# Optimization experiments

Measured on AMD Instinct MI355X. Metric: run time of the kernel, lower is better.

## Reference

```python
import jax, jax.numpy as jnp
import numpy as np

N_NODES = 50000
N_EDGES = 800000
IN_FEAT = 512
HIDDEN = 64
N_CLASS = 16


def setup_inputs() -> dict:
    key = jax.random.key(0)
    ks = jax.random.split(key, 8)
    x = jax.random.normal(ks[0], (N_NODES, IN_FEAT), dtype=jnp.float32)
    src = jax.random.randint(ks[1], (N_EDGES,), 0, N_NODES, dtype=jnp.int32)
    dst = jax.random.randint(ks[2], (N_EDGES,), 0, N_NODES, dtype=jnp.int32)
    edge_weight = jax.random.uniform(ks[3], (N_EDGES,), dtype=jnp.float32)
    # Glorot-ish init for layer weights (GraphConvolution weight + bias)
    W1 = jax.random.normal(ks[4], (IN_FEAT, HIDDEN), dtype=jnp.float32) * (1.0 / np.sqrt(IN_FEAT))
    b1 = jnp.zeros((HIDDEN,), dtype=jnp.float32)
    W2 = jax.random.normal(ks[5], (HIDDEN, N_CLASS), dtype=jnp.float32) * (1.0 / np.sqrt(HIDDEN))
    b2 = jnp.zeros((N_CLASS,), dtype=jnp.float32)
    return {"x": x, "src": src, "dst": dst, "edge_weight": edge_weight,
            "W1": W1, "b1": b1, "W2": W2, "b2": b2}


def _spmm(src, dst, edge_weight, h):
    # sparse adj @ h via gather + weighted segment_sum over destination nodes
    msgs = h[src] * edge_weight[:, None]          # [E, d]
    return jax.ops.segment_sum(msgs, dst, num_segments=N_NODES)  # [N, d]


def reference(x, src, dst, edge_weight, W1, b1, W2, b2):
    # Layer 1: relu(adj @ (x @ W1) + b1)
    h = _spmm(src, dst, edge_weight, x @ W1) + b1   # [N, HIDDEN]
    h = jax.nn.relu(h)
    # Dropout is identity at inference (predict uses training=False).
    # Layer 2: softmax(adj @ (h @ W2) + b2)
    logits = _spmm(src, dst, edge_weight, h @ W2) + b2  # [N, N_CLASS]
    return jax.nn.softmax(logits, axis=-1)
```

## Files before the change

kernel.cpp:

```cpp
#include <hip/hip_runtime.h>

#define IN_FEAT 512
#define HIDDEN 64
#define N_CLASS 16
#define CAP 64
#define EPT 4

typedef __attribute__((ext_vector_type(8))) short bf16x8;
typedef __attribute__((ext_vector_type(8))) unsigned short ushort8;
typedef __attribute__((ext_vector_type(4))) float f32x4;

struct EdgeRec { int s; float w; };

__device__ inline unsigned short f2bf(float f) {
    union { float f; unsigned int u; } x; x.f = f;
    unsigned int u = x.u + 0x7FFFu + ((x.u >> 16) & 1u);
    return (unsigned short)(u >> 16);
}

__global__ __launch_bounds__(256) void k_init(const float* __restrict__ W1,
                                              unsigned short* __restrict__ bfrag,
                                              int* __restrict__ deg, int n) {
    int bid = blockIdx.x;
    if (bid < 16) {
        int t = bid * 256 + threadIdx.x;
        int l = t & 63;
        int grp = t >> 6;
        int ct = grp & 3, kc = grp >> 2;
        int k0 = kc * 32 + (l >> 4) * 8;
        int col = ct * 16 + (l & 15);
        ushort8 v;
#pragma unroll
        for (int j = 0; j < 8; ++j) v[j] = f2bf(W1[(k0 + j) * HIDDEN + col]);
        ((ushort8*)bfrag)[t] = v;
    } else {
        int i = (bid - 16) * 256 + threadIdx.x;
        if (i < n) deg[i] = 0;
    }
}

__global__ __launch_bounds__(256) void k_fused(const float* __restrict__ x,
                                               const unsigned short* __restrict__ bfrag,
                                               float* __restrict__ h0,
                                               const int* __restrict__ src,
                                               const int* __restrict__ dst,
                                               const float* __restrict__ ew,
                                               int* __restrict__ deg,
                                               EdgeRec* __restrict__ recs,
                                               int n, int E, int gb) {
    int bid = blockIdx.x;
    int gid = bid >> 1;
    if ((bid & 1) == 0) {
        int wid  = gid * 4 + (threadIdx.x >> 6);
        int lane = threadIdx.x & 63;
        int r0 = wid * 16;
        if (r0 >= n) return;
        const float* xp = x + (size_t)(r0 + (lane & 15)) * IN_FEAT + (lane >> 4) * 8;

        bf16x8 afr[16];
#pragma unroll
        for (int kc = 0; kc < 16; ++kc) {
            f32x4 a0 = *(const f32x4*)(xp + kc * 32);
            f32x4 a1 = *(const f32x4*)(xp + kc * 32 + 4);
            bf16x8 a;
#pragma unroll
            for (int j = 0; j < 4; ++j) a[j] = (short)f2bf(a0[j]);
#pragma unroll
            for (int j = 0; j < 4; ++j) a[4 + j] = (short)f2bf(a1[j]);
            afr[kc] = a;
        }

        const bf16x8* B = (const bf16x8*)bfrag;
        f32x4 acc0 = {0,0,0,0}, acc1 = {0,0,0,0}, acc2 = {0,0,0,0}, acc3 = {0,0,0,0};
#pragma unroll
        for (int kc = 0; kc < 16; ++kc) {
            bf16x8 b0 = B[(kc * 4 + 0) * 64 + lane];
            bf16x8 b1 = B[(kc * 4 + 1) * 64 + lane];
            bf16x8 b2 = B[(kc * 4 + 2) * 64 + lane];
            bf16x8 b3 = B[(kc * 4 + 3) * 64 + lane];
            acc0 = __builtin_amdgcn_mfma_f32_16x16x32_bf16(afr[kc], b0, acc0, 0, 0, 0);
            acc1 = __builtin_amdgcn_mfma_f32_16x16x32_bf16(afr[kc], b1, acc1, 0, 0, 0);
            acc2 = __builtin_amdgcn_mfma_f32_16x16x32_bf16(afr[kc], b2, acc2, 0, 0, 0);
            acc3 = __builtin_amdgcn_mfma_f32_16x16x32_bf16(afr[kc], b3, acc3, 0, 0, 0);
        }

        int c = lane & 15;
        int rb = r0 + ((lane >> 4) << 2);
#pragma unroll
        for (int j = 0; j < 4; ++j) {
            float* o = h0 + (size_t)(rb + j) * HIDDEN;
            o[ 0 + c] = acc0[j];
            o[16 + c] = acc1[j];
            o[32 + c] = acc2[j];
            o[48 + c] = acc3[j];
        }
    } else {
        int base = gid * (256 * EPT) + threadIdx.x;
        int  dd[EPT], ss[EPT];
        float ww[EPT];
        bool pp[EPT];
#pragma unroll
        for (int k = 0; k < EPT; ++k) {
            int i = base + k * 256;
            pp[k] = (i < E);
            int j = pp[k] ? i : 0;
            dd[k] = dst[j];
            ss[k] = src[j];
            ww[k] = ew[j];
        }
        int rr[EPT];
#pragma unroll
        for (int k = 0; k < EPT; ++k)
            rr[k] = pp[k] ? atomicAdd(&deg[dd[k]], 1) : CAP;
#pragma unroll
        for (int k = 0; k < EPT; ++k) {
            if (rr[k] < CAP) {
                EdgeRec rec; rec.s = ss[k]; rec.w = ww[k];
                recs[(size_t)dd[k] * CAP + rr[k]] = rec;
            }
        }
    }
}

__global__ __launch_bounds__(256) void k_spmm1g2(const int* __restrict__ deg,
                                                 const EdgeRec* __restrict__ recs,
                                                 const float* __restrict__ h0,
                                                 const float* __restrict__ b1,
                                                 const float* __restrict__ W2,
                                                 float* __restrict__ h2, int n) {
    int wid  = blockIdx.x * 4 + (threadIdx.x >> 6);
    int lane = threadIdx.x & 63;
    if (wid >= n) return;
    int node = __builtin_amdgcn_readfirstlane(wid);
    int cnt = deg[node]; if (cnt > CAP) cnt = CAP;
    const EdgeRec* er = recs + (size_t)node * CAP;

    EdgeRec myr = {0, 0.f};
    if (lane < cnt) myr = er[lane];

    int f  = lane & 15;
    int kb = lane & 48;
    float bias = b1[lane];
    float w2r[16];
#pragma unroll
    for (int j = 0; j < 16; ++j) w2r[j] = W2[(kb + j) * N_CLASS + f];

    float acc = 0.f;
    for (int e = 0; e < cnt; e += 8) {
#define STEP(k)                                              \
        int   s##k = __shfl(myr.s, e + k, 64);               \
        float w##k = __shfl(myr.w, e + k, 64);               \
        bool  p##k = (e + k < cnt);                          \
        s##k = p##k ? s##k : 0;                              \
        w##k = p##k ? w##k : 0.f;                            \
        float g##k = h0[(size_t)s##k * HIDDEN + lane];
        STEP(0) STEP(1) STEP(2) STEP(3) STEP(4) STEP(5) STEP(6) STEP(7)
#undef STEP
        acc = fmaf(w0, g0, acc);
        acc = fmaf(w1, g1, acc);
        acc = fmaf(w2, g2, acc);
        acc = fmaf(w3, g3, acc);
        acc = fmaf(w4, g4, acc);
        acc = fmaf(w5, g5, acc);
        acc = fmaf(w6, g6, acc);
        acc = fmaf(w7, g7, acc);
    }
    float h1v = acc + bias;
    h1v = h1v > 0.f ? h1v : 0.f;

    float sum = 0.f;
#pragma unroll
    for (int j = 0; j < 16; ++j) {
        float hk = __shfl(h1v, kb + j, 64);
        sum = fmaf(hk, w2r[j], sum);
    }
    sum += __shfl_xor(sum, 16, 64);
    sum += __shfl_xor(sum, 32, 64);
    if (lane < 16) h2[(size_t)node * N_CLASS + lane] = sum;
}

__global__ __launch_bounds__(256) void k_spmm2(const int* __restrict__ deg,
                                               const EdgeRec* __restrict__ recs,
                                               const float* __restrict__ h2,
                                               const float* __restrict__ b2,
                                               float* __restrict__ out, int n) {
    int wid  = blockIdx.x * 4 + (threadIdx.x >> 6);
    int lane = threadIdx.x & 63;
    if (wid >= n) return;
    int node = __builtin_amdgcn_readfirstlane(wid);
    int cnt = deg[node]; if (cnt > CAP) cnt = CAP;
    const EdgeRec* er = recs + (size_t)node * CAP;

    EdgeRec myr = {0, 0.f};
    if (lane < cnt) myr = er[lane];

    int f = lane & 15;
    int q = lane >> 4;
    float bias = b2[f];

    float acc = 0.f;
#pragma unroll
    for (int i = 0; i < 16; ++i) {
        int e = 4 * i + q;
        int   s = __shfl(myr.s, e, 64);
        float w = __shfl(myr.w, e, 64);
        bool  p = (e < cnt);
        s = p ? s : 0;
        w = p ? w : 0.f;
        acc = fmaf(w, h2[(size_t)s * N_CLASS + f], acc);
    }
    acc += __shfl_xor(acc, 16, 64);
    acc += __shfl_xor(acc, 32, 64);

    float logit = acc + bias;
    float m = logit;
#pragma unroll
    for (int d = 1; d < 16; d <<= 1) m = fmaxf(m, __shfl_xor(m, d, 16));
    float ex = __expf(logit - m);
    float s = ex;
#pragma unroll
    for (int d = 1; d < 16; d <<= 1) s += __shfl_xor(s, d, 16);
    if (lane < 16) out[(size_t)node * N_CLASS + lane] = ex / s;
}

extern "C" void kernel_launch(void* const* d_in, const int* in_sizes, int n_in,
                              void* d_out, int out_size, void* d_ws, size_t ws_size,
                              hipStream_t stream) {
    const float* x   = (const float*)d_in[0];
    const int*   src = (const int*)d_in[1];
    const int*   dst = (const int*)d_in[2];
    const float* ew  = (const float*)d_in[3];
    const float* W1  = (const float*)d_in[4];
    const float* b1  = (const float*)d_in[5];
    const float* W2  = (const float*)d_in[6];
    const float* b2  = (const float*)d_in[7];
    float* out = (float*)d_out;

    int n = in_sizes[0] / IN_FEAT;
    int E = in_sizes[1];

    float*   h0   = (float*)d_ws;
    float*   h2   = h0 + (size_t)n * HIDDEN;
    EdgeRec* recs = (EdgeRec*)(h2 + (size_t)n * N_CLASS);
    int*     deg  = (int*)(recs + (size_t)n * CAP);
    unsigned short* bfrag = (unsigned short*)(deg + n);

    int nb = (n + 255) / 256;
    int gb = ((n + 15) / 16 + 3) / 4;
    int ebt = (E + 256 * EPT - 1) / (256 * EPT);
    int half = gb > ebt ? gb : ebt;

    k_init<<<16 + nb, 256, 0, stream>>>(W1, bfrag, deg, n);
    k_fused<<<2 * half, 256, 0, stream>>>(x, bfrag, h0, src, dst, ew, deg, recs, n, E, gb);
    k_spmm1g2<<<(n + 3) / 4, 256, 0, stream>>>(deg, recs, h0, b1, W2, h2, n);
    k_spmm2<<<(n + 3) / 4, 256, 0, stream>>>(deg, recs, h2, b2, out, n);
}
```

Measured before the change: 258.6 us.

## Split fused GEMM/bucketing kernel into separate launches and memset degree array

Splits the kernel that interleaved GEMM1 blocks with edge-bucketing blocks into two separate kernels launched one after the other. The degree array is now zeroed with hipMemsetAsync instead of inside the init kernel. This gives up the overlap of the compute-bound GEMM with the atomic-heavy bucketing and adds launches, in exchange for simpler per-kernel scheduling and occupancy.

```diff
diff --git a/kernel.cpp b/kernel.cpp
--- a/kernel.cpp
+++ b/kernel.cpp
@@ -18,106 +18,95 @@
     return (unsigned short)(u >> 16);
 }
 
-__global__ __launch_bounds__(256) void k_init(const float* __restrict__ W1,
-                                              unsigned short* __restrict__ bfrag,
-                                              int* __restrict__ deg, int n) {
-    int bid = blockIdx.x;
-    if (bid < 16) {
-        int t = bid * 256 + threadIdx.x;
-        int l = t & 63;
-        int grp = t >> 6;
-        int ct = grp & 3, kc = grp >> 2;
-        int k0 = kc * 32 + (l >> 4) * 8;
-        int col = ct * 16 + (l & 15);
-        ushort8 v;
-#pragma unroll
-        for (int j = 0; j < 8; ++j) v[j] = f2bf(W1[(k0 + j) * HIDDEN + col]);
-        ((ushort8*)bfrag)[t] = v;
-    } else {
-        int i = (bid - 16) * 256 + threadIdx.x;
-        if (i < n) deg[i] = 0;
-    }
-}
-
-__global__ __launch_bounds__(256) void k_fused(const float* __restrict__ x,
+__global__ __launch_bounds__(256) void k_prep(const float* __restrict__ W1,
+                                              unsigned short* __restrict__ bfrag) {
+    int t = blockIdx.x * 256 + threadIdx.x;
+    int l = t & 63;
+    int grp = t >> 6;
+    int ct = grp & 3, kc = grp >> 2;
+    int k0 = kc * 32 + (l >> 4) * 8;
+    int col = ct * 16 + (l & 15);
+    ushort8 v;
+#pragma unroll
+    for (int j = 0; j < 8; ++j) v[j] = f2bf(W1[(k0 + j) * HIDDEN + col]);
+    ((ushort8*)bfrag)[t] = v;
+}
+
+__global__ __launch_bounds__(256) void k_gemm1(const float* __restrict__ x,
                                                const unsigned short* __restrict__ bfrag,
-                                               float* __restrict__ h0,
-                                               const int* __restrict__ src,
-                                               const int* __restrict__ dst,
-                                               const float* __restrict__ ew,
-                                               int* __restrict__ deg,
-                                               EdgeRec* __restrict__ recs,
-                                               int n, int E, int gb) {
-    int bid = blockIdx.x;
-    int gid = bid >> 1;
-    if ((bid & 1) == 0) {
-        int wid  = gid * 4 + (threadIdx.x >> 6);
-        int lane = threadIdx.x & 63;
-        int r0 = wid * 16;
-        if (r0 >= n) return;
-        const float* xp = x + (size_t)(r0 + (lane & 15)) * IN_FEAT + (lane >> 4) * 8;
-
-        bf16x8 afr[16];
-#pragma unroll
-        for (int kc = 0; kc < 16; ++kc) {
-            f32x4 a0 = *(const f32x4*)(xp + kc * 32);
-            f32x4 a1 = *(const f32x4*)(xp + kc * 32 + 4);
-            bf16x8 a;
-#pragma unroll
-            for (int j = 0; j < 4; ++j) a[j] = (short)f2bf(a0[j]);
-#pragma unroll
-            for (int j = 0; j < 4; ++j) a[4 + j] = (short)f2bf(a1[j]);
-            afr[kc] = a;
-        }
-
-        const bf16x8* B = (const bf16x8*)bfrag;
-        f32x4 acc0 = {0,0,0,0}, acc1 = {0,0,0,0}, acc2 = {0,0,0,0}, acc3 = {0,0,0,0};
-#pragma unroll
-        for (int kc = 0; kc < 16; ++kc) {
-            bf16x8 b0 = B[(kc * 4 + 0) * 64 + lane];
-            bf16x8 b1 = B[(kc * 4 + 1) * 64 + lane];
-            bf16x8 b2 = B[(kc * 4 + 2) * 64 + lane];
-            bf16x8 b3 = B[(kc * 4 + 3) * 64 + lane];
-            acc0 = __builtin_amdgcn_mfma_f32_16x16x32_bf16(afr[kc], b0, acc0, 0, 0, 0);
-            acc1 = __builtin_amdgcn_mfma_f32_16x16x32_bf16(afr[kc], b1, acc1, 0, 0, 0);
-            acc2 = __builtin_amdgcn_mfma_f32_16x16x32_bf16(afr[kc], b2, acc2, 0, 0, 0);
-            acc3 = __builtin_amdgcn_mfma_f32_16x16x32_bf16(afr[kc], b3, acc3, 0, 0, 0);
-        }
-
-        int c = lane & 15;
-        int rb = r0 + ((lane >> 4) << 2);
-#pragma unroll
-        for (int j = 0; j < 4; ++j) {
-            float* o = h0 + (size_t)(rb + j) * HIDDEN;
-            o[ 0 + c] = acc0[j];
-            o[16 + c] = acc1[j];
-            o[32 + c] = acc2[j];
-            o[48 + c] = acc3[j];
-        }
-    } else {
-        int base = gid * (256 * EPT) + threadIdx.x;
-        int  dd[EPT], ss[EPT];
-        float ww[EPT];
-        bool pp[EPT];
-#pragma unroll
-        for (int k = 0; k < EPT; ++k) {
-            int i = base + k * 256;
-            pp[k] = (i < E);
-            int j = pp[k] ? i : 0;
-            dd[k] = dst[j];
-            ss[k] = src[j];
-            ww[k] = ew[j];
-        }
-        int rr[EPT];
-#pragma unroll
-        for (int k = 0; k < EPT; ++k)
-            rr[k] = pp[k] ? atomicAdd(&deg[dd[k]], 1) : CAP;
-#pragma unroll
-        for (int k = 0; k < EPT; ++k) {
-            if (rr[k] < CAP) {
-                EdgeRec rec; rec.s = ss[k]; rec.w = ww[k];
-                recs[(size_t)dd[k] * CAP + rr[k]] = rec;
-            }
+                                               float* __restrict__ h0, int n) {
+    int wid  = blockIdx.x * 4 + (threadIdx.x >> 6);
+    int lane = threadIdx.x & 63;
+    int r0 = wid * 16;
+    if (r0 >= n) return;
+    const float* xp = x + (size_t)(r0 + (lane & 15)) * IN_FEAT + (lane >> 4) * 8;
+
+    bf16x8 afr[16];
+#pragma unroll
+    for (int kc = 0; kc < 16; ++kc) {
+        f32x4 a0 = *(const f32x4*)(xp + kc * 32);
+        f32x4 a1 = *(const f32x4*)(xp + kc * 32 + 4);
+        bf16x8 a;
+#pragma unroll
+        for (int j = 0; j < 4; ++j) a[j] = (short)f2bf(a0[j]);
+#pragma unroll
+        for (int j = 0; j < 4; ++j) a[4 + j] = (short)f2bf(a1[j]);
+        afr[kc] = a;
+    }
+
+    const bf16x8* B = (const bf16x8*)bfrag;
+    f32x4 acc0 = {0,0,0,0}, acc1 = {0,0,0,0}, acc2 = {0,0,0,0}, acc3 = {0,0,0,0};
+#pragma unroll
+    for (int kc = 0; kc < 16; ++kc) {
+        bf16x8 b0 = B[(kc * 4 + 0) * 64 + lane];
+        bf16x8 b1 = B[(kc * 4 + 1) * 64 + lane];
+        bf16x8 b2 = B[(kc * 4 + 2) * 64 + lane];
+        bf16x8 b3 = B[(kc * 4 + 3) * 64 + lane];
+        acc0 = __builtin_amdgcn_mfma_f32_16x16x32_bf16(afr[kc], b0, acc0, 0, 0, 0);
+        acc1 = __builtin_amdgcn_mfma_f32_16x16x32_bf16(afr[kc], b1, acc1, 0, 0, 0);
+        acc2 = __builtin_amdgcn_mfma_f32_16x16x32_bf16(afr[kc], b2, acc2, 0, 0, 0);
+        acc3 = __builtin_amdgcn_mfma_f32_16x16x32_bf16(afr[kc], b3, acc3, 0, 0, 0);
+    }
+
+    int c = lane & 15;
+    int rb = r0 + ((lane >> 4) << 2);
+#pragma unroll
+    for (int j = 0; j < 4; ++j) {
+        float* o = h0 + (size_t)(rb + j) * HIDDEN;
+        o[ 0 + c] = acc0[j];
+        o[16 + c] = acc1[j];
+        o[32 + c] = acc2[j];
+        o[48 + c] = acc3[j];
+    }
+}
+
+__global__ __launch_bounds__(256) void k_bucket(const int* __restrict__ src,
+                                                const int* __restrict__ dst,
+                                                const float* __restrict__ ew,
+                                                int* __restrict__ deg,
+                                                EdgeRec* __restrict__ recs, int E) {
+    int base = blockIdx.x * (256 * EPT) + threadIdx.x;
+    int  dd[EPT], ss[EPT];
+    float ww[EPT];
+    bool pp[EPT];
+#pragma unroll
+    for (int k = 0; k < EPT; ++k) {
+        int i = base + k * 256;
+        pp[k] = (i < E);
+        int j = pp[k] ? i : 0;
+        dd[k] = dst[j];
+        ss[k] = src[j];
+        ww[k] = ew[j];
+    }
+    int rr[EPT];
+#pragma unroll
+    for (int k = 0; k < EPT; ++k)
+        rr[k] = pp[k] ? atomicAdd(&deg[dd[k]], 1) : CAP;
+#pragma unroll
+    for (int k = 0; k < EPT; ++k) {
+        if (rr[k] < CAP) {
+            EdgeRec rec; rec.s = ss[k]; rec.w = ww[k];
+            recs[(size_t)dd[k] * CAP + rr[k]] = rec;
         }
     }
 }
@@ -245,13 +234,13 @@
     int*     deg  = (int*)(recs + (size_t)n * CAP);
     unsigned short* bfrag = (unsigned short*)(deg + n);
 
-    int nb = (n + 255) / 256;
-    int gb = ((n + 15) / 16 + 3) / 4;
+    int gb  = ((n + 15) / 16 + 3) / 4;
     int ebt = (E + 256 * EPT - 1) / (256 * EPT);
-    int half = gb > ebt ? gb : ebt;
-
-    k_init<<<16 + nb, 256, 0, stream>>>(W1, bfrag, deg, n);
-    k_fused<<<2 * half, 256, 0, stream>>>(x, bfrag, h0, src, dst, ew, deg, recs, n, E, gb);
+
+    hipMemsetAsync(deg, 0, (size_t)n * sizeof(int), stream);
+    k_prep<<<16, 256, 0, stream>>>(W1, bfrag);
+    k_bucket<<<ebt, 256, 0, stream>>>(src, dst, ew, deg, recs, E);
+    k_gemm1<<<gb, 256, 0, stream>>>(x, bfrag, h0, n);
     k_spmm1g2<<<(n + 3) / 4, 256, 0, stream>>>(deg, recs, h0, b1, W2, h2, n);
     k_spmm2<<<(n + 3) / 4, 256, 0, stream>>>(deg, recs, h2, b2, out, n);
 }
```

New measurement: 288.2 us. 1.11x slower.
